# Kernel tuning notes

Measured on AMD Instinct MI355X. Metric: run time of the kernel, lower is better.

The kernel has to match this reference:

```python
import jax, jax.numpy as jnp
import numpy as np

B, H, W, C = 64, 56, 56, 256
ROUTES = 4
CONV_OUT = 64
BN_EPS = 1e-3  # keras BatchNormalization default epsilon


def setup_inputs() -> dict:
    key = jax.random.key(0)
    ks = jax.random.split(key, 8)
    inputs = jax.random.normal(ks[0], (B, H, W, C), jnp.float32)
    gamma = jnp.ones((C,), jnp.float32)
    beta = jnp.zeros((C,), jnp.float32)
    moving_mean = 0.1 * jax.random.normal(ks[1], (C,), jnp.float32)
    moving_var = jax.random.uniform(ks[2], (C,), jnp.float32, 0.5, 1.5)
    conv_w = 0.02 * jax.random.normal(ks[3], (3, 3, C, CONV_OUT), jnp.float32)  # HWIO
    conv_b = jnp.zeros((CONV_OUT,), jnp.float32)
    fc_w = 0.05 * jax.random.normal(ks[4], (CONV_OUT, ROUTES), jnp.float32)
    fc_b = jnp.zeros((ROUTES,), jnp.float32)
    return {"inputs": inputs, "gamma": gamma, "beta": beta,
            "moving_mean": moving_mean, "moving_var": moving_var,
            "conv_w": conv_w, "conv_b": conv_b, "fc_w": fc_w, "fc_b": fc_b}


def reference(inputs, gamma, beta, moving_mean, moving_var, conv_w, conv_b, fc_w, fc_b):
    # BatchNormalization in inference mode (training=None -> moving stats)
    rx = (inputs - moving_mean) * jax.lax.rsqrt(moving_var + BN_EPS) * gamma + beta
    # Conv2D(64, 3x3, stride 2, padding 'same'), NHWC / HWIO
    rx = jax.lax.conv_general_dilated(
        rx, conv_w, window_strides=(2, 2), padding="SAME",
        dimension_numbers=("NHWC", "HWIO", "NHWC")) + conv_b
    # GlobalAveragePooling2D -> [B, 64]
    rx = jnp.mean(rx, axis=(1, 2))
    # Dense(routes) -> routing logits [B, ROUTES]
    routing_x = rx @ fc_w + fc_b
    # choose_route: top-1 route, direct per-sample channel slice (no dense mask)
    route_width = C // ROUTES
    route = jnp.argmax(routing_x, axis=-1)  # [B]
    ch_idx = route[:, None] * route_width + jnp.arange(route_width)  # [B, rw]
    idx = ch_idx[:, None, None, :]  # [B,1,1,rw] broadcasts over H, W
    x = jnp.take_along_axis(inputs, idx, axis=3)  # [B, H, W, rw]
    return x, routing_x
```

## Files before the change

kernel.cpp:

```cpp
#include <hip/hip_runtime.h>

#define B 64
#define H 56
#define W 56
#define C 256
#define ROUTES 4
#define CONV_OUT 64
#define BN_EPS 0.001f
#define RW (C / ROUTES)

#define NSLOT 9
#define ACC_FLOATS (B * NSLOT * C)
#define X_SIZE ((long)B * H * W * RW)

#define ROWS_PER_BLK 4
#define CHUNKS (H / ROWS_PER_BLK)

__device__ __forceinline__ void f4add(float4& a, const float4& v) {
    a.x += v.x; a.y += v.y; a.z += v.z; a.w += v.w;
}

__global__ __launch_bounds__(256) void k_reduce(const float* __restrict__ x,
                                                float* __restrict__ acc) {
    int blk = blockIdx.x;
    int b = blk / CHUNKS;
    int h0 = (blk % CHUNKS) * ROWS_PER_BLK;
    int tid = threadIdx.x;
    int cg = tid & 63;
    int wg = tid >> 6;
    int wp = wg & 1;

    const float4* xv = (const float4*)x;

    float4 s0 = {0,0,0,0};
    float4 s1 = {0,0,0,0};
    float4 c0e = {0,0,0,0};
    float4 c0o = {0,0,0,0};
    float4 r0  = {0,0,0,0};
    float4 x00 = {0,0,0,0};

    for (int hh = 0; hh < ROWS_PER_BLK; ++hh) {
        int h = h0 + hh;
        long base = ((long)(b * H + h) * W) * (C / 4) + cg;
        float4 rs = {0,0,0,0};
        for (int w = wg; w < W; w += 4) {
            float4 v = xv[base + (long)w * (C / 4)];
            f4add(rs, v);
            if (wg == 0 && w == 0) {
                if ((h & 1) == 0) f4add(c0e, v); else f4add(c0o, v);
                if (h == 0) x00 = v;
            }
        }
        if (h & 1) f4add(s1, rs); else f4add(s0, rs);
        if (h == 0) r0 = rs;
    }

    float* accb = acc + (long)b * NSLOT * C;
    int c = cg * 4;
    #define AT4(slot, v) { float* p = accb + (slot) * C + c; \
        atomicAdd(p+0, (v).x); atomicAdd(p+1, (v).y); \
        atomicAdd(p+2, (v).z); atomicAdd(p+3, (v).w); }

    AT4(0 + wp, s0);
    AT4(2 + wp, s1);
    if (wg == 0) { AT4(4, c0e); AT4(5, c0o); }
    if (h0 == 0) {
        AT4(6 + wp, r0);
        if (wg == 0) {
            float* p = accb + 8 * C + c;
            p[0] = x00.x; p[1] = x00.y; p[2] = x00.z; p[3] = x00.w;
        }
    }
    #undef AT4
}

__global__ __launch_bounds__(256) void k_route(const float* __restrict__ acc,
                                               const float* __restrict__ gamma,
                                               const float* __restrict__ beta,
                                               const float* __restrict__ mmean,
                                               const float* __restrict__ mvar,
                                               const float* __restrict__ conv_w,
                                               const float* __restrict__ conv_b,
                                               const float* __restrict__ fc_w,
                                               const float* __restrict__ fc_b,
                                               float* __restrict__ out_routing,
                                               int* __restrict__ route) {
    __shared__ float tl[9][C];
    __shared__ float part[4][CONV_OUT];
    __shared__ float cm[CONV_OUT];
    __shared__ float rxs[ROUTES];

    int b = blockIdx.x;
    int c = threadIdx.x;
    const float* ab = acc + (long)b * NSLOT * C;

    float See = ab[0*C+c], Seo = ab[1*C+c], Soe = ab[2*C+c], Soo = ab[3*C+c];
    float c0e = ab[4*C+c], c0o = ab[5*C+c];
    float r0e = ab[6*C+c], r0o = ab[7*C+c], x00 = ab[8*C+c];

    float a  = gamma[c] * rsqrtf(mvar[c] + BN_EPS);
    float bb = beta[c] - mmean[c] * a;

    float Sx[9] = { See,             Seo,             See - c0e,
                    Soe,             Soo,             Soe - c0o,
                    See - r0e,       Seo - r0o,       See - r0e - c0e + x00 };
    const float cnt[9] = { 784.f, 784.f, 756.f,
                           784.f, 784.f, 756.f,
                           756.f, 756.f, 729.f };
    for (int k = 0; k < 9; ++k) tl[k][c] = a * Sx[k] + bb * cnt[k];
    __syncthreads();

    int o = threadIdx.x & 63;
    int g = threadIdx.x >> 6;
    float p = 0.f;
    for (int cc = g * 64; cc < g * 64 + 64; ++cc) {
        #pragma unroll
        for (int k = 0; k < 9; ++k)
            p += tl[k][cc] * conv_w[(k * C + cc) * CONV_OUT + o];
    }
    part[g][o] = p;
    __syncthreads();

    if (threadIdx.x < CONV_OUT) {
        int o2 = threadIdx.x;
        float s = part[0][o2] + part[1][o2] + part[2][o2] + part[3][o2];
        cm[o2] = s * (1.f / 784.f) + conv_b[o2];
    }
    __syncthreads();

    if (threadIdx.x < ROUTES) {
        int r = threadIdx.x;
        float s = fc_b[r];
        for (int o2 = 0; o2 < CONV_OUT; ++o2) s += cm[o2] * fc_w[o2 * ROUTES + r];
        rxs[r] = s;
        out_routing[b * ROUTES + r] = s;
    }
    __syncthreads();

    if (threadIdx.x == 0) {
        int best = 0;
        for (int r = 1; r < ROUTES; ++r) if (rxs[r] > rxs[best]) best = r;
        route[b] = best;
    }
}

__global__ __launch_bounds__(256) void k_gather(const float* __restrict__ x,
                                                const int* __restrict__ route,
                                                float* __restrict__ out) {
    long idx = (long)blockIdx.x * blockDim.x + threadIdx.x;
    int j = (int)(idx & 15);
    long pixel = idx >> 4;
    int b = (int)(pixel / (H * W));
    const float4* xv = (const float4*)x;
    float4 v = xv[pixel * (C / 4) + (long)route[b] * (RW / 4) + j];
    ((float4*)out)[idx] = v;
}

extern "C" void kernel_launch(void* const* d_in, const int* in_sizes, int n_in,
                              void* d_out, int out_size, void* d_ws, size_t ws_size,
                              hipStream_t stream) {
    const float* inputs = (const float*)d_in[0];
    const float* gamma  = (const float*)d_in[1];
    const float* beta   = (const float*)d_in[2];
    const float* mmean  = (const float*)d_in[3];
    const float* mvar   = (const float*)d_in[4];
    const float* conv_w = (const float*)d_in[5];
    const float* conv_b = (const float*)d_in[6];
    const float* fc_w   = (const float*)d_in[7];
    const float* fc_b   = (const float*)d_in[8];

    float* out   = (float*)d_out;
    float* acc   = (float*)d_ws;
    int*   route = (int*)((char*)d_ws + ACC_FLOATS * sizeof(float));

    hipMemsetAsync(d_ws, 0, ACC_FLOATS * sizeof(float), stream);

    k_reduce<<<B * CHUNKS, 256, 0, stream>>>(inputs, acc);
    k_route<<<B, 256, 0, stream>>>(acc, gamma, beta, mmean, mvar,
                                   conv_w, conv_b, fc_w, fc_b,
                                   out + X_SIZE, route);
    long n4 = X_SIZE / 4;
    k_gather<<<(int)(n4 / 256), 256, 0, stream>>>(inputs, route, out);
}
```

Measured before the change: 378.8 us.

## Replace atomic accumulation with per-block partial sums reduced in route kernel

The reduce kernel now handles one row pair per block, issuing all 28 float4 loads up front, and writes per-block per-wave partial sums to a workspace with plain stores. This removes the float atomics and the memset. The route kernel then sums the partials across the 28 row pairs. The extra workspace traffic and the serial reduction loop in the 64-block route kernel add cost, and register use grows from holding 28 float4 values.

```diff
diff --git a/kernel.cpp b/kernel.cpp
--- a/kernel.cpp
+++ b/kernel.cpp
@@ -8,73 +8,78 @@
 #define CONV_OUT 64
 #define BN_EPS 0.001f
 #define RW (C / ROUTES)
-
-#define NSLOT 9
-#define ACC_FLOATS (B * NSLOT * C)
 #define X_SIZE ((long)B * H * W * RW)
 
-#define ROWS_PER_BLK 4
-#define CHUNKS (H / ROWS_PER_BLK)
+#define PAIRS (H / 2)
+
+#define S4 ((long)B * PAIRS * 8 * C)
+#define SC ((long)B * PAIRS * 2 * C)
+#define SR ((long)B * 4 * C)
+#define SX ((long)B * C)
+#define OFF4 0L
+#define OFFC (OFF4 + S4)
+#define OFFR (OFFC + SC)
+#define OFFX (OFFR + SR)
+#define WS_FLOATS (OFFX + SX)
 
 __device__ __forceinline__ void f4add(float4& a, const float4& v) {
     a.x += v.x; a.y += v.y; a.z += v.z; a.w += v.w;
 }
 
 __global__ __launch_bounds__(256) void k_reduce(const float* __restrict__ x,
-                                                float* __restrict__ acc) {
+                                                float* __restrict__ ws) {
     int blk = blockIdx.x;
-    int b = blk / CHUNKS;
-    int h0 = (blk % CHUNKS) * ROWS_PER_BLK;
+    int b = blk / PAIRS;
+    int j = blk % PAIRS;
     int tid = threadIdx.x;
     int cg = tid & 63;
     int wg = tid >> 6;
-    int wp = wg & 1;
 
     const float4* xv = (const float4*)x;
-
-    float4 s0 = {0,0,0,0};
-    float4 s1 = {0,0,0,0};
-    float4 c0e = {0,0,0,0};
-    float4 c0o = {0,0,0,0};
-    float4 r0  = {0,0,0,0};
-    float4 x00 = {0,0,0,0};
-
-    for (int hh = 0; hh < ROWS_PER_BLK; ++hh) {
-        int h = h0 + hh;
-        long base = ((long)(b * H + h) * W) * (C / 4) + cg;
-        float4 rs = {0,0,0,0};
-        for (int w = wg; w < W; w += 4) {
-            float4 v = xv[base + (long)w * (C / 4)];
-            f4add(rs, v);
-            if (wg == 0 && w == 0) {
-                if ((h & 1) == 0) f4add(c0e, v); else f4add(c0o, v);
-                if (h == 0) x00 = v;
-            }
+    long row0 = ((long)(b * H + 2 * j) * W) * (C / 4) + cg;
+    long row1 = row0 + (long)W * (C / 4);
+
+    float4 r0[14], r1[14];
+    #pragma unroll
+    for (int i = 0; i < 14; ++i) r0[i] = xv[row0 + (long)(wg + 4 * i) * (C / 4)];
+    #pragma unroll
+    for (int i = 0; i < 14; ++i) r1[i] = xv[row1 + (long)(wg + 4 * i) * (C / 4)];
+
+    float4 s0 = {0,0,0,0}, s1 = {0,0,0,0};
+    {
+        float4 a = {0,0,0,0}, bq = {0,0,0,0};
+        #pragma unroll
+        for (int i = 0; i < 14; i += 2) { f4add(a, r0[i]); f4add(bq, r0[i+1]); }
+        f4add(s0, a); f4add(s0, bq);
+    }
+    {
+        float4 a = {0,0,0,0}, bq = {0,0,0,0};
+        #pragma unroll
+        for (int i = 0; i < 14; i += 2) { f4add(a, r1[i]); f4add(bq, r1[i+1]); }
+        f4add(s1, a); f4add(s1, bq);
+    }
+
+    int c4 = cg;
+    float4* acc4 = (float4*)(ws + OFF4) + ((long)blk * 8 + wg) * (C / 4) + c4;
+    acc4[0]             = s0;
+    acc4[4 * (C / 4)]   = s1;
+
+    if (wg == 0) {
+        float4* accc = (float4*)(ws + OFFC) + ((long)blk * 2) * (C / 4) + c4;
+        accc[0]       = r0[0];
+        accc[C / 4]   = r1[0];
+    }
+    if (j == 0) {
+        float4* accr = (float4*)(ws + OFFR) + ((long)b * 4 + wg) * (C / 4) + c4;
+        accr[0] = s0;
+        if (wg == 0) {
+            float4* accx = (float4*)(ws + OFFX) + (long)b * (C / 4) + c4;
+            accx[0] = r0[0];
         }
-        if (h & 1) f4add(s1, rs); else f4add(s0, rs);
-        if (h == 0) r0 = rs;
-    }
-
-    float* accb = acc + (long)b * NSLOT * C;
-    int c = cg * 4;
-    #define AT4(slot, v) { float* p = accb + (slot) * C + c; \
-        atomicAdd(p+0, (v).x); atomicAdd(p+1, (v).y); \
-        atomicAdd(p+2, (v).z); atomicAdd(p+3, (v).w); }
-
-    AT4(0 + wp, s0);
-    AT4(2 + wp, s1);
-    if (wg == 0) { AT4(4, c0e); AT4(5, c0o); }
-    if (h0 == 0) {
-        AT4(6 + wp, r0);
-        if (wg == 0) {
-            float* p = accb + 8 * C + c;
-            p[0] = x00.x; p[1] = x00.y; p[2] = x00.z; p[3] = x00.w;
-        }
-    }
-    #undef AT4
-}
-
-__global__ __launch_bounds__(256) void k_route(const float* __restrict__ acc,
+    }
+}
+
+__global__ __launch_bounds__(256) void k_route(const float* __restrict__ ws,
                                                const float* __restrict__ gamma,
                                                const float* __restrict__ beta,
                                                const float* __restrict__ mmean,
@@ -92,11 +97,25 @@
 
     int b = blockIdx.x;
     int c = threadIdx.x;
-    const float* ab = acc + (long)b * NSLOT * C;
-
-    float See = ab[0*C+c], Seo = ab[1*C+c], Soe = ab[2*C+c], Soo = ab[3*C+c];
-    float c0e = ab[4*C+c], c0o = ab[5*C+c];
-    float r0e = ab[6*C+c], r0o = ab[7*C+c], x00 = ab[8*C+c];
+
+    float See = 0, Seo = 0, Soe = 0, Soo = 0, c0e = 0, c0o = 0;
+    const float* a4 = ws + OFF4 + (long)b * PAIRS * 8 * C;
+    for (int j = 0; j < PAIRS; ++j) {
+        const float* p = a4 + (long)j * 8 * C + c;
+        See += p[0 * C] + p[2 * C];
+        Seo += p[1 * C] + p[3 * C];
+        Soe += p[4 * C] + p[6 * C];
+        Soo += p[5 * C] + p[7 * C];
+    }
+    const float* pc = ws + OFFC + (long)b * PAIRS * 2 * C;
+    for (int j = 0; j < PAIRS; ++j) {
+        c0e += pc[(long)(2 * j) * C + c];
+        c0o += pc[(long)(2 * j + 1) * C + c];
+    }
+    const float* pr = ws + OFFR + (long)b * 4 * C;
+    float r0e = pr[0 * C + c] + pr[2 * C + c];
+    float r0o = pr[1 * C + c] + pr[3 * C + c];
+    float x00 = ws[OFFX + (long)b * C + c];
 
     float a  = gamma[c] * rsqrtf(mvar[c] + BN_EPS);
     float bb = beta[c] - mmean[c] * a;
@@ -107,6 +126,7 @@
     const float cnt[9] = { 784.f, 784.f, 756.f,
                            784.f, 784.f, 756.f,
                            756.f, 756.f, 729.f };
+    #pragma unroll
     for (int k = 0; k < 9; ++k) tl[k][c] = a * Sx[k] + bb * cnt[k];
     __syncthreads();
 
@@ -170,13 +190,11 @@
     const float* fc_b   = (const float*)d_in[8];
 
     float* out   = (float*)d_out;
-    float* acc   = (float*)d_ws;
-    int*   route = (int*)((char*)d_ws + ACC_FLOATS * sizeof(float));
-
-    hipMemsetAsync(d_ws, 0, ACC_FLOATS * sizeof(float), stream);
-
-    k_reduce<<<B * CHUNKS, 256, 0, stream>>>(inputs, acc);
-    k_route<<<B, 256, 0, stream>>>(acc, gamma, beta, mmean, mvar,
+    float* ws    = (float*)d_ws;
+    int*   route = (int*)((char*)d_ws + WS_FLOATS * sizeof(float));
+
+    k_reduce<<<B * PAIRS, 256, 0, stream>>>(inputs, ws);
+    k_route<<<B, 256, 0, stream>>>(ws, gamma, beta, mmean, mvar,
                                    conv_w, conv_b, fc_w, fc_b,
                                    out + X_SIZE, route);
     long n4 = X_SIZE / 4;
```

New measurement: 356.7 us. 5.8% less time.

## Replace atomic accumulation with per-row partial sums and drop memset

Applied to the files above, without the earlier changes.

The reduction kernel now launches one block per image row, loads all 14 columns per thread up front, combines even and odd column sums through shared memory, and writes per-row partials plus the first-column value to workspace with plain stores. The route kernel then sums these partials over rows itself. This removes the float atomics and the workspace memset. The gather uses nontemporal stores for the output. In exchange the workspace grows and the serial per-block reduction in k_route gets longer.

```diff
diff --git a/kernel.cpp b/kernel.cpp
--- a/kernel.cpp
+++ b/kernel.cpp
@@ -8,73 +8,51 @@
 #define CONV_OUT 64
 #define BN_EPS 0.001f
 #define RW (C / ROUTES)
-
-#define NSLOT 9
-#define ACC_FLOATS (B * NSLOT * C)
 #define X_SIZE ((long)B * H * W * RW)
 
-#define ROWS_PER_BLK 4
-#define CHUNKS (H / ROWS_PER_BLK)
+#define WS_FLOATS ((long)B * H * 3 * C)
+
+typedef float floatx4 __attribute__((ext_vector_type(4)));
 
 __device__ __forceinline__ void f4add(float4& a, const float4& v) {
     a.x += v.x; a.y += v.y; a.z += v.z; a.w += v.w;
 }
 
 __global__ __launch_bounds__(256) void k_reduce(const float* __restrict__ x,
-                                                float* __restrict__ acc) {
+                                                float* __restrict__ ws) {
     int blk = blockIdx.x;
-    int b = blk / CHUNKS;
-    int h0 = (blk % CHUNKS) * ROWS_PER_BLK;
     int tid = threadIdx.x;
     int cg = tid & 63;
     int wg = tid >> 6;
-    int wp = wg & 1;
 
     const float4* xv = (const float4*)x;
+    long base = (long)blk * W * (C / 4) + cg;
 
-    float4 s0 = {0,0,0,0};
-    float4 s1 = {0,0,0,0};
-    float4 c0e = {0,0,0,0};
-    float4 c0o = {0,0,0,0};
-    float4 r0  = {0,0,0,0};
-    float4 x00 = {0,0,0,0};
+    float4 v[14];
+    #pragma unroll
+    for (int i = 0; i < 14; ++i) v[i] = xv[base + (long)(wg + 4 * i) * (C / 4)];
 
-    for (int hh = 0; hh < ROWS_PER_BLK; ++hh) {
-        int h = h0 + hh;
-        long base = ((long)(b * H + h) * W) * (C / 4) + cg;
-        float4 rs = {0,0,0,0};
-        for (int w = wg; w < W; w += 4) {
-            float4 v = xv[base + (long)w * (C / 4)];
-            f4add(rs, v);
-            if (wg == 0 && w == 0) {
-                if ((h & 1) == 0) f4add(c0e, v); else f4add(c0o, v);
-                if (h == 0) x00 = v;
-            }
-        }
-        if (h & 1) f4add(s1, rs); else f4add(s0, rs);
-        if (h == 0) r0 = rs;
+    float4 a = {0,0,0,0}, b4 = {0,0,0,0};
+    #pragma unroll
+    for (int i = 0; i < 14; i += 2) { f4add(a, v[i]); f4add(b4, v[i + 1]); }
+    f4add(a, b4);
+
+    __shared__ float4 lds[4][64];
+    lds[wg][cg] = a;
+
+    float4* w3 = (float4*)ws + (long)blk * 3 * (C / 4);
+    if (wg == 0) w3[2 * (C / 4) + cg] = v[0];
+    __syncthreads();
+    if (wg == 0) {
+        float4 e = lds[0][cg]; f4add(e, lds[2][cg]);
+        w3[cg] = e;
+    } else if (wg == 1) {
+        float4 o = lds[1][cg]; f4add(o, lds[3][cg]);
+        w3[C / 4 + cg] = o;
     }
-
-    float* accb = acc + (long)b * NSLOT * C;
-    int c = cg * 4;
-    #define AT4(slot, v) { float* p = accb + (slot) * C + c; \
-        atomicAdd(p+0, (v).x); atomicAdd(p+1, (v).y); \
-        atomicAdd(p+2, (v).z); atomicAdd(p+3, (v).w); }
-
-    AT4(0 + wp, s0);
-    AT4(2 + wp, s1);
-    if (wg == 0) { AT4(4, c0e); AT4(5, c0o); }
-    if (h0 == 0) {
-        AT4(6 + wp, r0);
-        if (wg == 0) {
-            float* p = accb + 8 * C + c;
-            p[0] = x00.x; p[1] = x00.y; p[2] = x00.z; p[3] = x00.w;
-        }
-    }
-    #undef AT4
 }
 
-__global__ __launch_bounds__(256) void k_route(const float* __restrict__ acc,
+__global__ __launch_bounds__(256) void k_route(const float* __restrict__ ws,
                                                const float* __restrict__ gamma,
                                                const float* __restrict__ beta,
                                                const float* __restrict__ mmean,
@@ -92,11 +70,18 @@
 
     int b = blockIdx.x;
     int c = threadIdx.x;
-    const float* ab = acc + (long)b * NSLOT * C;
 
-    float See = ab[0*C+c], Seo = ab[1*C+c], Soe = ab[2*C+c], Soo = ab[3*C+c];
-    float c0e = ab[4*C+c], c0o = ab[5*C+c];
-    float r0e = ab[6*C+c], r0o = ab[7*C+c], x00 = ab[8*C+c];
+    const float* base = ws + (long)b * H * 3 * C;
+    float See = 0, Seo = 0, Soe = 0, Soo = 0, c0e = 0, c0o = 0;
+    for (int h = 0; h < H; h += 2) {
+        const float* pe = base + (long)h * 3 * C;
+        const float* po = pe + 3 * C;
+        See += pe[c];          Seo += pe[C + c];     c0e += pe[2 * C + c];
+        Soe += po[c];          Soo += po[C + c];     c0o += po[2 * C + c];
+    }
+    float r0e = base[c];
+    float r0o = base[C + c];
+    float x00 = base[2 * C + c];
 
     float a  = gamma[c] * rsqrtf(mvar[c] + BN_EPS);
     float bb = beta[c] - mmean[c] * a;
@@ -107,6 +92,7 @@
     const float cnt[9] = { 784.f, 784.f, 756.f,
                            784.f, 784.f, 756.f,
                            756.f, 756.f, 729.f };
+    #pragma unroll
     for (int k = 0; k < 9; ++k) tl[k][c] = a * Sx[k] + bb * cnt[k];
     __syncthreads();
 
@@ -151,9 +137,9 @@
     int j = (int)(idx & 15);
     long pixel = idx >> 4;
     int b = (int)(pixel / (H * W));
-    const float4* xv = (const float4*)x;
-    float4 v = xv[pixel * (C / 4) + (long)route[b] * (RW / 4) + j];
-    ((float4*)out)[idx] = v;
+    const floatx4* xv = (const floatx4*)x;
+    floatx4 v = xv[pixel * (C / 4) + (long)route[b] * (RW / 4) + j];
+    __builtin_nontemporal_store(v, &((floatx4*)out)[idx]);
 }
 
 extern "C" void kernel_launch(void* const* d_in, const int* in_sizes, int n_in,
@@ -170,13 +156,11 @@
     const float* fc_b   = (const float*)d_in[8];
 
     float* out   = (float*)d_out;
-    float* acc   = (float*)d_ws;
-    int*   route = (int*)((char*)d_ws + ACC_FLOATS * sizeof(float));
+    float* ws    = (float*)d_ws;
+    int*   route = (int*)((char*)d_ws + WS_FLOATS * sizeof(float));
 
-    hipMemsetAsync(d_ws, 0, ACC_FLOATS * sizeof(float), stream);
-
-    k_reduce<<<B * CHUNKS, 256, 0, stream>>>(inputs, acc);
-    k_route<<<B, 256, 0, stream>>>(acc, gamma, beta, mmean, mvar,
+    k_reduce<<<B * H, 256, 0, stream>>>(inputs, ws);
+    k_route<<<B, 256, 0, stream>>>(ws, gamma, beta, mmean, mvar,
                                    conv_w, conv_b, fc_w, fc_b,
                                    out + X_SIZE, route);
     long n4 = X_SIZE / 4;
```

Result: faster. 354.0 us (-6.5%).
